# Kernel optimization log

Hardware: AMD Instinct MI355X
Metric: run time of the kernel (lower is better)

## Reference

```python
import jax, jax.numpy as jnp
import numpy as np

H, C = 4, 32  # heads, per-head channels
EPS = 1e-5


def setup_inputs() -> dict:
    key = jax.random.key(0)
    ks = jax.random.split(key, 12)
    N, E, IN = 100000, 1600000, 16
    lut_idx = jnp.arange(1024, dtype=jnp.int32)
    x = jax.random.normal(ks[0], (N, IN), dtype=jnp.float32)
    # LUT flag column: exactly the lut_idx nodes have value 1.0 (matches x[:,15]==1.0 mask)
    x = x.at[:, 15].set(0.0).at[lut_idx, 15].set(1.0)
    edge_index = jax.random.randint(ks[1], (2, E), 0, N, dtype=jnp.int64)
    s = 0.1
    return {
        "x": x,
        "edge_index": edge_index,
        "lut_idx": lut_idx,
        "W_lin": jax.random.normal(ks[2], (IN, H * C), dtype=jnp.float32) * s,
        "att_src": jax.random.normal(ks[3], (H, C), dtype=jnp.float32) * s,
        "att_dst": jax.random.normal(ks[4], (H, C), dtype=jnp.float32) * s,
        "bias_gat": jnp.zeros((H * C,), dtype=jnp.float32),
        "gamma": jnp.ones((H * C,), dtype=jnp.float32),
        "beta": jnp.zeros((H * C,), dtype=jnp.float32),
        "W1": jax.random.normal(ks[5], (H * C, 32), dtype=jnp.float32) * s,
        "b1": jnp.zeros((32,), dtype=jnp.float32),
        "W2": jax.random.normal(ks[6], (32, 1), dtype=jnp.float32) * s,
        "b2": jnp.zeros((1,), dtype=jnp.float32),
    }


def gat_conv(x, edge_index, W_lin, att_src, att_dst, bias_gat):
    N = x.shape[0]
    # add self-loops (PyG GATConv default)
    loops = jnp.arange(N, dtype=edge_index.dtype)
    src = jnp.concatenate([edge_index[0], loops])
    dst = jnp.concatenate([edge_index[1], loops])
    h = (x @ W_lin).reshape(N, H, C)                      # [N,H,C]
    a_src = (h * att_src[None]).sum(-1)                   # [N,H]
    a_dst = (h * att_dst[None]).sum(-1)                   # [N,H]
    e = jax.nn.leaky_relu(a_src[src] + a_dst[dst], 0.2)   # [Etot,H]
    m = jax.ops.segment_max(e, dst, num_segments=N)       # stable softmax per dst
    e = jnp.exp(e - m[dst])
    denom = jax.ops.segment_sum(e, dst, num_segments=N)
    alpha = e / denom[dst]                                # [Etot,H]
    msg = h[src] * alpha[:, :, None]                      # [Etot,H,C]
    out = jax.ops.segment_sum(msg, dst, num_segments=N)   # [N,H,C]
    return out.reshape(N, H * C) + bias_gat


def reference(x, edge_index, lut_idx, W_lin, att_src, att_dst, bias_gat,
              gamma, beta, W1, b1, W2, b2):
    h = gat_conv(x, edge_index, W_lin, att_src, att_dst, bias_gat)
    # BatchNorm over nodes (training-mode batch stats, biased var, eps=1e-5)
    mean = h.mean(axis=0)
    var = h.var(axis=0)
    h = (h - mean) / jnp.sqrt(var + EPS) * gamma + beta
    h = jax.nn.relu(h)
    emb = h[lut_idx]                                      # masked LUT nodes
    z = jax.nn.leaky_relu(emb @ W1 + b1, 0.01)            # Dropout is identity in eval
    out = z @ W2 + b2                                     # [n_lut, 1]
    return jnp.squeeze(out, axis=0) if out.shape[0] == 1 else out
```

## Files before the change

### kernel.cpp

```cpp
#include <hip/hip_runtime.h>
#include <hip/hip_fp16.h>
#include <cstdint>
#include <cstring>

typedef unsigned int uint;

#define BSHIFT 8
#define NBUCK 512
#define TILE 4096
#define SCAT_T 512
#define FUSE_T 1024
#define SORT_CAP 5120

__device__ __forceinline__ float leaky02(float x) { return x > 0.f ? x : 0.2f * x; }
__device__ __forceinline__ float bflo(uint u) { return __uint_as_float(u << 16); }
__device__ __forceinline__ float bfhi(uint u) { return __uint_as_float(u & 0xffff0000u); }

__device__ __forceinline__ uint pack_bf16x2(float a, float b) {
    uint ua = __float_as_uint(a), ub = __float_as_uint(b);
    ua += 0x7fffu + ((ua >> 16) & 1u);
    ub += 0x7fffu + ((ub >> 16) & 1u);
    return (ua >> 16) | (ub & 0xffff0000u);
}

__device__ __forceinline__ uint packh2(float a, float b) {
    __half ha = __float2half_rn(a), hb = __float2half_rn(b);
    unsigned short ua, ub;
    memcpy(&ua, &ha, 2);
    memcpy(&ub, &hb, 2);
    return (uint)ua | ((uint)ub << 16);
}

__device__ __forceinline__ float h2f_sel(uint2 xw, int head) {
    uint wrd = (head & 2) ? xw.y : xw.x;
    unsigned short us = (unsigned short)((head & 1) ? (wrd >> 16) : (wrd & 0xffffu));
    __half hh; memcpy(&hh, &us, 2);
    return __half2float(hh);
}

__global__ void k_linear(const float* __restrict__ x, const float* __restrict__ W,
                         const float* __restrict__ att_s, const float* __restrict__ att_d,
                         uint* __restrict__ h, float* __restrict__ a_src,
                         float* __restrict__ a_dst, int* __restrict__ cursor,
                         float* __restrict__ sums, float* __restrict__ sumsq,
                         unsigned char* __restrict__ flags, int N) {
    int tid = threadIdx.x;
    __shared__ float sx[32][16];
    __shared__ float sWs[64], sWd[64];
    int j = tid & 63;
    int sub = tid >> 6;
    int n0 = blockIdx.x * 32;

    if (blockIdx.x == 0) {
        cursor[tid] = 0; cursor[tid + 256] = 0;
        if (tid < 128) sums[tid] = 0.f;
        else sumsq[tid - 128] = 0.f;
    }
    if (tid < 32 && n0 + tid < N) flags[n0 + tid] = 0;

    float2 wreg[16];
#pragma unroll
    for (int k = 0; k < 16; k++) wreg[k] = ((const float2*)(W + k * 128))[j];

    if (tid < 128) {
        int row = tid >> 2;
        if (n0 + row < N)
            ((float4*)sx)[tid] = ((const float4*)(x + (size_t)n0 * 16))[tid];
    } else if (tid < 192) {
        int t = tid - 128;
        int k = t >> 2, hh = t & 3;
        float s1 = 0.f, s2 = 0.f;
        for (int c = 0; c < 32; c++) {
            float wv = W[k * 128 + hh * 32 + c];
            s1 += wv * att_s[hh * 32 + c];
            s2 += wv * att_d[hh * 32 + c];
        }
        sWs[t] = s1;
        sWd[t] = s2;
    }
    __syncthreads();

#pragma unroll
    for (int i = 0; i < 8; i++) {
        int loc = sub + i * 4;
        int n = n0 + loc;
        if (n >= N) break;
        float acc0 = 0.f, acc1 = 0.f;
#pragma unroll
        for (int k = 0; k < 16; k++) {
            float xk = sx[loc][k];
            acc0 += xk * wreg[k].x;
            acc1 += xk * wreg[k].y;
        }
        h[(size_t)n * 64 + j] = pack_bf16x2(acc0, acc1);
    }

    int loc2 = tid >> 3, hh = (tid >> 1) & 3, sd = tid & 1;
    int n2 = n0 + loc2;
    if (n2 < N) {
        const float* Wm = sd ? sWd : sWs;
        float acc = 0.f;
#pragma unroll
        for (int k = 0; k < 16; k++) acc += sx[loc2][k] * Wm[k * 4 + hh];
        if (sd) a_dst[n2 * 4 + hh] = acc;
        else    a_src[n2 * 4 + hh] = acc;
    }
}

__global__ void kb_scatter(const int* __restrict__ src, const int* __restrict__ dst, int E,
                           int* __restrict__ cursor, uint* __restrict__ pairs,
                           const int* __restrict__ lut, int nlut,
                           unsigned char* __restrict__ flags) {
    __shared__ int tileCnt[NBUCK], tileCnt2[NBUCK], tileOff[NBUCK], gbase[NBUCK];
    __shared__ int wsum[8], wbase[8];
    __shared__ uint lp[TILE];
    __shared__ unsigned short lb[TILE];
    int tid = threadIdx.x;
    int l = tid & 63, w = tid >> 6;
    int t0 = blockIdx.x * TILE;
    if (blockIdx.x == 0) {
        for (int k = tid; k < nlut; k += SCAT_T) flags[lut[k]] = 1;
    }
    tileCnt[tid] = 0;
    tileCnt2[tid] = 0;
    __syncthreads();
    int dreg[8], sreg[8];
#pragma unroll
    for (int j = 0; j < 8; j++) {
        int idx = t0 + j * SCAT_T + tid;
        if (idx < E) {
            dreg[j] = dst[idx];
            sreg[j] = src[idx];
            atomicAdd(&tileCnt[dreg[j] >> BSHIFT], 1);
        } else dreg[j] = -1;
    }
    __syncthreads();
    int v = tileCnt[tid];
    int s = v;
#pragma unroll
    for (int off = 1; off < 64; off <<= 1) {
        int t = __shfl_up(s, off);
        if (l >= off) s += t;
    }
    if (l == 63) wsum[w] = s;
    __syncthreads();
    if (tid < 8) {
        int b = 0;
        for (int i = 0; i < tid; i++) b += wsum[i];
        wbase[tid] = b;
    }
    __syncthreads();
    int ex = s - v + wbase[w];
    tileOff[tid] = ex;
    if (v > 0) gbase[tid] = atomicAdd(&cursor[tid], v);
    __syncthreads();
#pragma unroll
    for (int j = 0; j < 8; j++) {
        if (dreg[j] >= 0) {
            int bk = dreg[j] >> BSHIFT;
            int r = atomicAdd(&tileCnt2[bk], 1);
            int pos = tileOff[bk] + r;
            lp[pos] = ((uint)sreg[j] << BSHIFT) | (uint)(dreg[j] & 255);
            lb[pos] = (unsigned short)bk;
        }
    }
    __syncthreads();
    int tot = min(TILE, E - t0);
    for (int k = tid; k < tot; k += SCAT_T) {
        int bk = lb[k];
        int lpos = gbase[bk] + (k - tileOff[bk]);
        if (lpos < SORT_CAP)
            pairs[(size_t)bk * SORT_CAP + lpos] = lp[k];
    }
}

__global__ void __launch_bounds__(1024, 8) kb_sortgat(
                           const uint* __restrict__ pairs, const int* __restrict__ cursor,
                           const float* __restrict__ a_src, const float* __restrict__ a_dst,
                           const uint* __restrict__ h, const float* __restrict__ bias,
                           const unsigned char* __restrict__ flags,
                           uint* __restrict__ hagg,
                           float* __restrict__ sums, float* __restrict__ sumsq, int N) {
    __shared__ int cnt[256], off0[256], degl[256];
    __shared__ int wsum[4], wbase[4];
    __shared__ uint lcode[SORT_CAP];
    __shared__ uint2 wlds[SORT_CAP];
    __shared__ float4 sad[256];
    int tid = threadIdx.x;
    int l = tid & 63, w = tid >> 6;
    int b = blockIdx.x;
    int n0 = b << BSHIFT;
    int nn = min(256, N - n0);
    int ebase = b * SORT_CAP;
    int ecnt = cursor[b];
    if (ecnt > SORT_CAP) ecnt = SORT_CAP;
    if (tid < 256) cnt[tid] = 0;
    if (tid < nn) sad[tid] = ((const float4*)a_dst)[n0 + tid];
    __syncthreads();
    for (int k = tid; k < ecnt; k += FUSE_T)
        atomicAdd(&cnt[pairs[ebase + k] & 255], 1);
    __syncthreads();
    int v = (tid < 256) ? cnt[tid] : 0;
    int s = v;
#pragma unroll
    for (int off = 1; off < 64; off <<= 1) {
        int t = __shfl_up(s, off);
        if (l >= off) s += t;
    }
    if (tid < 256 && l == 63) wsum[w] = s;
    __syncthreads();
    if (tid < 4) {
        int base = 0;
        for (int i = 0; i < tid; i++) base += wsum[i];
        wbase[tid] = base;
    }
    __syncthreads();
    if (tid < 256) {
        off0[tid] = s - v + wbase[w];
        degl[tid] = v;
    }
    __syncthreads();
    if (tid < 256) cnt[tid] = 0;
    __syncthreads();
    for (int k = tid; k < ecnt; k += FUSE_T) {
        uint p = pairs[ebase + k];
        int ln = p & 255;
        int src = (int)(p >> BSHIFT);
        int r = atomicAdd(&cnt[ln], 1);
        int pos = off0[ln] + r;
        lcode[pos] = (uint)src;
        float4 as = ((const float4*)a_src)[src];
        float4 ad = sad[ln];
        wlds[pos] = make_uint2(
            packh2(__expf(leaky02(as.x + ad.x)), __expf(leaky02(as.y + ad.y))),
            packh2(__expf(leaky02(as.z + ad.z)), __expf(leaky02(as.w + ad.w))));
    }
    __syncthreads();
    int q = l >> 4;
    int l16 = l & 15;
    int head = l16 >> 2;
    float4 b0 = ((const float4*)bias)[2 * l16];
    float4 b1 = ((const float4*)bias)[2 * l16 + 1];
    float sv[8], sq[8];
#pragma unroll
    for (int j = 0; j < 8; j++) { sv[j] = 0.f; sq[j] = 0.f; }
    for (int pass = 0; pass < 4; pass++) {
        int ln = pass * 64 + w * 4 + q;
        if (ln >= nn) continue;
        int d = n0 + ln;
        int ebs = off0[ln];
        int deg = degl[ln];
        float asv = a_src[d * 4 + head];
        float adv = ((const float*)sad)[ln * 4 + head];
        float wslf = __expf(leaky02(asv + adv));
        uint4 u = ((const uint4*)(h + (size_t)d * 64))[l16];
        float sum = wslf;
        float2 a01 = make_float2(wslf * bflo(u.x), wslf * bfhi(u.x));
        float2 a23 = make_float2(wslf * bflo(u.y), wslf * bfhi(u.y));
        float2 a45 = make_float2(wslf * bflo(u.z), wslf * bfhi(u.z));
        float2 a67 = make_float2(wslf * bflo(u.w), wslf * bfhi(u.w));

        int i = 0;
        for (; i + 3 < deg; i += 4) {
            uint p0 = lcode[ebs + i];
            uint p1 = lcode[ebs + i + 1];
            uint p2 = lcode[ebs + i + 2];
            uint p3 = lcode[ebs + i + 3];
            uint2 x0 = wlds[ebs + i];
            uint2 x1 = wlds[ebs + i + 1];
            uint2 x2 = wlds[ebs + i + 2];
            uint2 x3 = wlds[ebs + i + 3];
            float w0 = h2f_sel(x0, head);
            float w1 = h2f_sel(x1, head);
            float w2 = h2f_sel(x2, head);
            float w3 = h2f_sel(x3, head);
            uint4 u0 = ((const uint4*)(h + (size_t)p0 * 64))[l16];
            uint4 u1 = ((const uint4*)(h + (size_t)p1 * 64))[l16];
            uint4 u2 = ((const uint4*)(h + (size_t)p2 * 64))[l16];
            uint4 u3 = ((const uint4*)(h + (size_t)p3 * 64))[l16];
            sum += (w0 + w1) + (w2 + w3);
            float2 w02 = {w0, w0}, w12 = {w1, w1}, w22 = {w2, w2}, w32 = {w3, w3};
            a01 += make_float2(bflo(u0.x), bfhi(u0.x)) * w02
                 + make_float2(bflo(u1.x), bfhi(u1.x)) * w12
                 + make_float2(bflo(u2.x), bfhi(u2.x)) * w22
                 + make_float2(bflo(u3.x), bfhi(u3.x)) * w32;
            a23 += make_float2(bflo(u0.y), bfhi(u0.y)) * w02
                 + make_float2(bflo(u1.y), bfhi(u1.y)) * w12
                 + make_float2(bflo(u2.y), bfhi(u2.y)) * w22
                 + make_float2(bflo(u3.y), bfhi(u3.y)) * w32;
            a45 += make_float2(bflo(u0.z), bfhi(u0.z)) * w02
                 + make_float2(bflo(u1.z), bfhi(u1.z)) * w12
                 + make_float2(bflo(u2.z), bfhi(u2.z)) * w22
                 + make_float2(bflo(u3.z), bfhi(u3.z)) * w32;
            a67 += make_float2(bflo(u0.w), bfhi(u0.w)) * w02
                 + make_float2(bflo(u1.w), bfhi(u1.w)) * w12
                 + make_float2(bflo(u2.w), bfhi(u2.w)) * w22
                 + make_float2(bflo(u3.w), bfhi(u3.w)) * w32;
        }
        for (; i < deg; i++) {
            uint p0 = lcode[ebs + i];
            float w0 = h2f_sel(wlds[ebs + i], head);
            uint4 u0 = ((const uint4*)(h + (size_t)p0 * 64))[l16];
            sum += w0;
            float2 w02 = {w0, w0};
            a01 += make_float2(bflo(u0.x), bfhi(u0.x)) * w02;
            a23 += make_float2(bflo(u0.y), bfhi(u0.y)) * w02;
            a45 += make_float2(bflo(u0.z), bfhi(u0.z)) * w02;
            a67 += make_float2(bflo(u0.w), bfhi(u0.w)) * w02;
        }
        float inv = 1.f / sum;
        float v0 = a01.x * inv + b0.x;
        float v1 = a01.y * inv + b0.y;
        float v2 = a23.x * inv + b0.z;
        float v3 = a23.y * inv + b0.w;
        float v4 = a45.x * inv + b1.x;
        float v5 = a45.y * inv + b1.y;
        float v6 = a67.x * inv + b1.z;
        float v7 = a67.y * inv + b1.w;
        sv[0] += v0; sq[0] += v0 * v0;
        sv[1] += v1; sq[1] += v1 * v1;
        sv[2] += v2; sq[2] += v2 * v2;
        sv[3] += v3; sq[3] += v3 * v3;
        sv[4] += v4; sq[4] += v4 * v4;
        sv[5] += v5; sq[5] += v5 * v5;
        sv[6] += v6; sq[6] += v6 * v6;
        sv[7] += v7; sq[7] += v7 * v7;
        if (flags[d]) {
            uint4 o;
            o.x = pack_bf16x2(v0, v1);
            o.y = pack_bf16x2(v2, v3);
            o.z = pack_bf16x2(v4, v5);
            o.w = pack_bf16x2(v6, v7);
            ((uint4*)(hagg + (size_t)d * 64))[l16] = o;
        }
    }
    __syncthreads();
#pragma unroll
    for (int j = 0; j < 8; j++) {
        sv[j] += __shfl_xor(sv[j], 16);
        sv[j] += __shfl_xor(sv[j], 32);
        sq[j] += __shfl_xor(sq[j], 16);
        sq[j] += __shfl_xor(sq[j], 32);
    }
    float* red = (float*)lcode;
    if (l < 16) {
#pragma unroll
        for (int j = 0; j < 8; j++) {
            red[(w * 16 + l) * 16 + j] = sv[j];
            red[(w * 16 + l) * 16 + 8 + j] = sq[j];
        }
    }
    __syncthreads();
    if (tid < 256) {
        int lg = tid >> 4, j = tid & 15;
        float tot = 0.f;
#pragma unroll
        for (int ww = 0; ww < 16; ww++) tot += red[(ww * 16 + lg) * 16 + j];
        if (j < 8) atomicAdd(&sums[lg * 8 + j], tot);
        else       atomicAdd(&sumsq[lg * 8 + j - 8], tot);
    }
}

__global__ void k_mlp(const uint* __restrict__ hagg, const int* __restrict__ lut,
                      const float* __restrict__ sums, const float* __restrict__ sumsq,
                      const float* __restrict__ gamma, const float* __restrict__ beta,
                      const float* __restrict__ W1, const float* __restrict__ b1,
                      const float* __restrict__ W2, const float* __restrict__ b2,
                      float* __restrict__ out, int N, int nlut) {
    int blk = blockIdx.x;
    if (blk >= nlut) return;
    int node = lut[blk];
    int lane = threadIdx.x;
    __shared__ float v[128];
    float invN = 1.f / (float)N;
    uint u = hagg[(size_t)node * 64 + lane];
    int c0 = 2 * lane, c1 = 2 * lane + 1;
    {
        float mean = sums[c0] * invN;
        float var = sumsq[c0] * invN - mean * mean;
        float val = (bflo(u) - mean) / sqrtf(var + 1e-5f) * gamma[c0] + beta[c0];
        v[c0] = fmaxf(val, 0.f);
        mean = sums[c1] * invN;
        var = sumsq[c1] * invN - mean * mean;
        val = (bfhi(u) - mean) / sqrtf(var + 1e-5f) * gamma[c1] + beta[c1];
        v[c1] = fmaxf(val, 0.f);
    }
    __syncthreads();
    float r = 0.f;
    if (lane < 32) {
        float z = b1[lane];
        for (int c = 0; c < 128; c++) z += v[c] * W1[c * 32 + lane];
        z = z > 0.f ? z : 0.01f * z;
        r = z * W2[lane];
    }
#pragma unroll
    for (int off = 16; off >= 1; off >>= 1) r += __shfl_xor(r, off);
    if (lane == 0) out[blk] = r + b2[0];
}

extern "C" void kernel_launch(void* const* d_in, const int* in_sizes, int n_in,
                              void* d_out, int out_size, void* d_ws, size_t ws_size,
                              hipStream_t stream) {
    const float* x     = (const float*)d_in[0];
    const int*   edges = (const int*)d_in[1];
    const int*   lut   = (const int*)d_in[2];
    const float* W_lin = (const float*)d_in[3];
    const float* att_s = (const float*)d_in[4];
    const float* att_d = (const float*)d_in[5];
    const float* bias  = (const float*)d_in[6];
    const float* gamma = (const float*)d_in[7];
    const float* beta  = (const float*)d_in[8];
    const float* W1    = (const float*)d_in[9];
    const float* b1    = (const float*)d_in[10];
    const float* W2    = (const float*)d_in[11];
    const float* b2    = (const float*)d_in[12];

    int N = in_sizes[0] / 16;
    int E = in_sizes[1] / 2;
    int nlut = in_sizes[2];
    int B = (N + 255) >> BSHIFT;

    const int* esrc = edges;
    const int* edst = edges + E;

    char* ws = (char*)d_ws;
    size_t off = 0;
    auto alloc = [&](size_t bytes) -> void* {
        void* p = ws + off;
        off += (bytes + 255) & ~(size_t)255;
        return p;
    };
    uint*  h       = (uint*)alloc((size_t)N * 64 * 4);
    uint*  hagg    = (uint*)alloc((size_t)N * 64 * 4);
    float* a_src   = (float*)alloc((size_t)N * 4 * 4);
    float* a_dst   = (float*)alloc((size_t)N * 4 * 4);
    uint*  pairs   = (uint*)alloc((size_t)B * SORT_CAP * 4);
    int*   cursor  = (int*)alloc((size_t)NBUCK * 4);
    float* sums    = (float*)alloc(128 * 4);
    float* sumsq   = (float*)alloc(128 * 4);
    unsigned char* flags = (unsigned char*)alloc((size_t)N);

    k_linear<<<(N + 31) / 32, 256, 0, stream>>>(x, W_lin, att_s, att_d, h,
                                                a_src, a_dst, cursor, sums, sumsq,
                                                flags, N);
    kb_scatter<<<(E + TILE - 1) / TILE, SCAT_T, 0, stream>>>(esrc, edst, E, cursor, pairs,
                                                             lut, nlut, flags);
    kb_sortgat<<<B, FUSE_T, 0, stream>>>(pairs, cursor, a_src, a_dst, h, bias,
                                         flags, hagg, sums, sumsq, N);
    k_mlp<<<nlut, 64, 0, stream>>>(hagg, lut, sums, sumsq, gamma, beta, W1, b1, W2, b2,
                                   (float*)d_out, N, nlut);
}
```

Baseline: 211.3 us.

## Fuse linear and edge-scatter kernels into one launch, zero buffers via memset

Merges the node linear projection and the edge bucket-scatter into a single kernel whose blocks branch on blockIdx, so the two independent phases run concurrently in one launch instead of two serialized ones. Zeroing of cursor, sums and flags moves into a hipMemsetAsync, since the scatter blocks can no longer rely on a prior kernel to clear them. The sort/aggregate kernel also stages the bias in shared memory and cuts the gather unroll from 4 to 2 to ease register pressure. The merged kernel uses a larger shared-memory footprint per block, and the linear part now handles 64 nodes per 512-thread block.

After: 190.5 us. 9.8% less time.

```diff
diff --git a/kernel.cpp b/kernel.cpp
--- a/kernel.cpp
+++ b/kernel.cpp
@@ -8,8 +8,8 @@
 #define BSHIFT 8
 #define NBUCK 512
 #define TILE 4096
-#define SCAT_T 512
 #define FUSE_T 1024
+#define LS_T 512
 #define SORT_CAP 5120
 
 __device__ __forceinline__ float leaky02(float x) { return x > 0.f ? x : 0.2f * x; }
@@ -38,139 +38,131 @@
     return __half2float(hh);
 }
 
-__global__ void k_linear(const float* __restrict__ x, const float* __restrict__ W,
-                         const float* __restrict__ att_s, const float* __restrict__ att_d,
-                         uint* __restrict__ h, float* __restrict__ a_src,
-                         float* __restrict__ a_dst, int* __restrict__ cursor,
-                         float* __restrict__ sums, float* __restrict__ sumsq,
-                         unsigned char* __restrict__ flags, int N) {
+__global__ void k_linscat(const float* __restrict__ x, const float* __restrict__ W,
+                          const float* __restrict__ att_s, const float* __restrict__ att_d,
+                          uint* __restrict__ h, float* __restrict__ a_src,
+                          float* __restrict__ a_dst,
+                          const int* __restrict__ src, const int* __restrict__ dst, int E,
+                          int* __restrict__ cursor, uint* __restrict__ pairs,
+                          const int* __restrict__ lut, int nlut,
+                          unsigned char* __restrict__ flags, int N, int Lb) {
     int tid = threadIdx.x;
-    __shared__ float sx[32][16];
-    __shared__ float sWs[64], sWd[64];
-    int j = tid & 63;
-    int sub = tid >> 6;
-    int n0 = blockIdx.x * 32;
-
-    if (blockIdx.x == 0) {
-        cursor[tid] = 0; cursor[tid + 256] = 0;
-        if (tid < 128) sums[tid] = 0.f;
-        else sumsq[tid - 128] = 0.f;
-    }
-    if (tid < 32 && n0 + tid < N) flags[n0 + tid] = 0;
-
-    float2 wreg[16];
-#pragma unroll
-    for (int k = 0; k < 16; k++) wreg[k] = ((const float2*)(W + k * 128))[j];
-
-    if (tid < 128) {
-        int row = tid >> 2;
-        if (n0 + row < N)
-            ((float4*)sx)[tid] = ((const float4*)(x + (size_t)n0 * 16))[tid];
-    } else if (tid < 192) {
-        int t = tid - 128;
-        int k = t >> 2, hh = t & 3;
-        float s1 = 0.f, s2 = 0.f;
-        for (int c = 0; c < 32; c++) {
-            float wv = W[k * 128 + hh * 32 + c];
-            s1 += wv * att_s[hh * 32 + c];
-            s2 += wv * att_d[hh * 32 + c];
-        }
-        sWs[t] = s1;
-        sWd[t] = s2;
-    }
-    __syncthreads();
-
-#pragma unroll
-    for (int i = 0; i < 8; i++) {
-        int loc = sub + i * 4;
-        int n = n0 + loc;
-        if (n >= N) break;
-        float acc0 = 0.f, acc1 = 0.f;
-#pragma unroll
-        for (int k = 0; k < 16; k++) {
-            float xk = sx[loc][k];
-            acc0 += xk * wreg[k].x;
-            acc1 += xk * wreg[k].y;
-        }
-        h[(size_t)n * 64 + j] = pack_bf16x2(acc0, acc1);
-    }
-
-    int loc2 = tid >> 3, hh = (tid >> 1) & 3, sd = tid & 1;
-    int n2 = n0 + loc2;
-    if (n2 < N) {
-        const float* Wm = sd ? sWd : sWs;
-        float acc = 0.f;
-#pragma unroll
-        for (int k = 0; k < 16; k++) acc += sx[loc2][k] * Wm[k * 4 + hh];
-        if (sd) a_dst[n2 * 4 + hh] = acc;
-        else    a_src[n2 * 4 + hh] = acc;
-    }
-}
-
-__global__ void kb_scatter(const int* __restrict__ src, const int* __restrict__ dst, int E,
-                           int* __restrict__ cursor, uint* __restrict__ pairs,
-                           const int* __restrict__ lut, int nlut,
-                           unsigned char* __restrict__ flags) {
-    __shared__ int tileCnt[NBUCK], tileCnt2[NBUCK], tileOff[NBUCK], gbase[NBUCK];
-    __shared__ int wsum[8], wbase[8];
-    __shared__ uint lp[TILE];
-    __shared__ unsigned short lb[TILE];
-    int tid = threadIdx.x;
-    int l = tid & 63, w = tid >> 6;
-    int t0 = blockIdx.x * TILE;
-    if (blockIdx.x == 0) {
-        for (int k = tid; k < nlut; k += SCAT_T) flags[lut[k]] = 1;
-    }
-    tileCnt[tid] = 0;
-    tileCnt2[tid] = 0;
-    __syncthreads();
-    int dreg[8], sreg[8];
-#pragma unroll
-    for (int j = 0; j < 8; j++) {
-        int idx = t0 + j * SCAT_T + tid;
-        if (idx < E) {
-            dreg[j] = dst[idx];
-            sreg[j] = src[idx];
-            atomicAdd(&tileCnt[dreg[j] >> BSHIFT], 1);
-        } else dreg[j] = -1;
-    }
-    __syncthreads();
-    int v = tileCnt[tid];
-    int s = v;
-#pragma unroll
-    for (int off = 1; off < 64; off <<= 1) {
-        int t = __shfl_up(s, off);
-        if (l >= off) s += t;
-    }
-    if (l == 63) wsum[w] = s;
-    __syncthreads();
-    if (tid < 8) {
-        int b = 0;
-        for (int i = 0; i < tid; i++) b += wsum[i];
-        wbase[tid] = b;
-    }
-    __syncthreads();
-    int ex = s - v + wbase[w];
-    tileOff[tid] = ex;
-    if (v > 0) gbase[tid] = atomicAdd(&cursor[tid], v);
-    __syncthreads();
-#pragma unroll
-    for (int j = 0; j < 8; j++) {
-        if (dreg[j] >= 0) {
-            int bk = dreg[j] >> BSHIFT;
-            int r = atomicAdd(&tileCnt2[bk], 1);
-            int pos = tileOff[bk] + r;
-            lp[pos] = ((uint)sreg[j] << BSHIFT) | (uint)(dreg[j] & 255);
-            lb[pos] = (unsigned short)bk;
-        }
-    }
-    __syncthreads();
-    int tot = min(TILE, E - t0);
-    for (int k = tid; k < tot; k += SCAT_T) {
-        int bk = lb[k];
-        int lpos = gbase[bk] + (k - tileOff[bk]);
-        if (lpos < SORT_CAP)
-            pairs[(size_t)bk * SORT_CAP + lpos] = lp[k];
+    if (blockIdx.x < Lb) {
+        __shared__ float sx[64][16];
+        __shared__ float sWs[64], sWd[64];
+        int j = tid & 63;
+        int sub = tid >> 6;
+        int n0 = blockIdx.x * 64;
+
+        float2 wreg[16];
+#pragma unroll
+        for (int k = 0; k < 16; k++) wreg[k] = ((const float2*)(W + k * 128))[j];
+
+        if (tid < 256) {
+            int row = tid >> 2;
+            if (n0 + row < N)
+                ((float4*)sx)[tid] = ((const float4*)(x + (size_t)n0 * 16))[tid];
+        } else if (tid < 320) {
+            int t = tid - 256;
+            int k = t >> 2, hh = t & 3;
+            float s1 = 0.f, s2 = 0.f;
+            for (int c = 0; c < 32; c++) {
+                float wv = W[k * 128 + hh * 32 + c];
+                s1 += wv * att_s[hh * 32 + c];
+                s2 += wv * att_d[hh * 32 + c];
+            }
+            sWs[t] = s1;
+            sWd[t] = s2;
+        }
+        __syncthreads();
+
+#pragma unroll
+        for (int i = 0; i < 8; i++) {
+            int loc = sub + i * 8;
+            int n = n0 + loc;
+            if (n >= N) break;
+            float acc0 = 0.f, acc1 = 0.f;
+#pragma unroll
+            for (int k = 0; k < 16; k++) {
+                float xk = sx[loc][k];
+                acc0 += xk * wreg[k].x;
+                acc1 += xk * wreg[k].y;
+            }
+            h[(size_t)n * 64 + j] = pack_bf16x2(acc0, acc1);
+        }
+
+        int loc2 = tid >> 3, hh = (tid >> 1) & 3, sd = tid & 1;
+        int n2 = n0 + loc2;
+        if (n2 < N) {
+            const float* Wm = sd ? sWd : sWs;
+            float acc = 0.f;
+#pragma unroll
+            for (int k = 0; k < 16; k++) acc += sx[loc2][k] * Wm[k * 4 + hh];
+            if (sd) a_dst[n2 * 4 + hh] = acc;
+            else    a_src[n2 * 4 + hh] = acc;
+        }
+    } else {
+        __shared__ int tileCnt[NBUCK], tileCnt2[NBUCK], tileOff[NBUCK], gbase[NBUCK];
+        __shared__ int wsum[8], wbase[8];
+        __shared__ uint lp[TILE];
+        __shared__ unsigned short lb[TILE];
+        int bid = blockIdx.x - Lb;
+        int l = tid & 63, w = tid >> 6;
+        int t0 = bid * TILE;
+        if (bid == 0) {
+            for (int k = tid; k < nlut; k += LS_T) flags[lut[k]] = 1;
+        }
+        tileCnt[tid] = 0;
+        tileCnt2[tid] = 0;
+        __syncthreads();
+        int dreg[8], sreg[8];
+#pragma unroll
+        for (int jj = 0; jj < 8; jj++) {
+            int idx = t0 + jj * LS_T + tid;
+            if (idx < E) {
+                dreg[jj] = dst[idx];
+                sreg[jj] = src[idx];
+                atomicAdd(&tileCnt[dreg[jj] >> BSHIFT], 1);
+            } else dreg[jj] = -1;
+        }
+        __syncthreads();
+        int v = tileCnt[tid];
+        int s = v;
+#pragma unroll
+        for (int off = 1; off < 64; off <<= 1) {
+            int t = __shfl_up(s, off);
+            if (l >= off) s += t;
+        }
+        if (l == 63) wsum[w] = s;
+        __syncthreads();
+        if (tid < 8) {
+            int b = 0;
+            for (int i = 0; i < tid; i++) b += wsum[i];
+            wbase[tid] = b;
+        }
+        __syncthreads();
+        int ex = s - v + wbase[w];
+        tileOff[tid] = ex;
+        if (v > 0) gbase[tid] = atomicAdd(&cursor[tid], v);
+        __syncthreads();
+#pragma unroll
+        for (int jj = 0; jj < 8; jj++) {
+            if (dreg[jj] >= 0) {
+                int bk = dreg[jj] >> BSHIFT;
+                int r = atomicAdd(&tileCnt2[bk], 1);
+                int pos = tileOff[bk] + r;
+                lp[pos] = ((uint)sreg[jj] << BSHIFT) | (uint)(dreg[jj] & 255);
+                lb[pos] = (unsigned short)bk;
+            }
+        }
+        __syncthreads();
+        int tot = min(TILE, E - t0);
+        for (int k = tid; k < tot; k += LS_T) {
+            int bk = lb[k];
+            int lpos = gbase[bk] + (k - tileOff[bk]);
+            if (lpos < SORT_CAP)
+                pairs[(size_t)bk * SORT_CAP + lpos] = lp[k];
+        }
     }
 }
 
@@ -186,6 +178,7 @@
     __shared__ uint lcode[SORT_CAP];
     __shared__ uint2 wlds[SORT_CAP];
     __shared__ float4 sad[256];
+    __shared__ float4 sbias[32];
     int tid = threadIdx.x;
     int l = tid & 63, w = tid >> 6;
     int b = blockIdx.x;
@@ -196,6 +189,7 @@
     if (ecnt > SORT_CAP) ecnt = SORT_CAP;
     if (tid < 256) cnt[tid] = 0;
     if (tid < nn) sad[tid] = ((const float4*)a_dst)[n0 + tid];
+    if (tid >= 992) sbias[tid - 992] = ((const float4*)bias)[tid - 992];
     __syncthreads();
     for (int k = tid; k < ecnt; k += FUSE_T)
         atomicAdd(&cnt[pairs[ebase + k] & 255], 1);
@@ -239,8 +233,6 @@
     int q = l >> 4;
     int l16 = l & 15;
     int head = l16 >> 2;
-    float4 b0 = ((const float4*)bias)[2 * l16];
-    float4 b1 = ((const float4*)bias)[2 * l16 + 1];
     float sv[8], sq[8];
 #pragma unroll
     for (int j = 0; j < 8; j++) { sv[j] = 0.f; sq[j] = 0.f; }
@@ -261,43 +253,25 @@
         float2 a67 = make_float2(wslf * bflo(u.w), wslf * bfhi(u.w));
 
         int i = 0;
-        for (; i + 3 < deg; i += 4) {
+        for (; i + 1 < deg; i += 2) {
             uint p0 = lcode[ebs + i];
             uint p1 = lcode[ebs + i + 1];
-            uint p2 = lcode[ebs + i + 2];
-            uint p3 = lcode[ebs + i + 3];
-            uint2 x0 = wlds[ebs + i];
-            uint2 x1 = wlds[ebs + i + 1];
-            uint2 x2 = wlds[ebs + i + 2];
-            uint2 x3 = wlds[ebs + i + 3];
-            float w0 = h2f_sel(x0, head);
-            float w1 = h2f_sel(x1, head);
-            float w2 = h2f_sel(x2, head);
-            float w3 = h2f_sel(x3, head);
+            float w0 = h2f_sel(wlds[ebs + i], head);
+            float w1 = h2f_sel(wlds[ebs + i + 1], head);
             uint4 u0 = ((const uint4*)(h + (size_t)p0 * 64))[l16];
             uint4 u1 = ((const uint4*)(h + (size_t)p1 * 64))[l16];
-            uint4 u2 = ((const uint4*)(h + (size_t)p2 * 64))[l16];
-            uint4 u3 = ((const uint4*)(h + (size_t)p3 * 64))[l16];
-            sum += (w0 + w1) + (w2 + w3);
-            float2 w02 = {w0, w0}, w12 = {w1, w1}, w22 = {w2, w2}, w32 = {w3, w3};
+            sum += w0 + w1;
+            float2 w02 = {w0, w0}, w12 = {w1, w1};
             a01 += make_float2(bflo(u0.x), bfhi(u0.x)) * w02
-                 + make_float2(bflo(u1.x), bfhi(u1.x)) * w12
-                 + make_float2(bflo(u2.x), bfhi(u2.x)) * w22
-                 + make_float2(bflo(u3.x), bfhi(u3.x)) * w32;
+                 + make_float2(bflo(u1.x), bfhi(u1.x)) * w12;
             a23 += make_float2(bflo(u0.y), bfhi(u0.y)) * w02
-                 + make_float2(bflo(u1.y), bfhi(u1.y)) * w12
-                 + make_float2(bflo(u2.y), bfhi(u2.y)) * w22
-                 + make_float2(bflo(u3.y), bfhi(u3.y)) * w32;
+                 + make_float2(bflo(u1.y), bfhi(u1.y)) * w12;
             a45 += make_float2(bflo(u0.z), bfhi(u0.z)) * w02
-                 + make_float2(bflo(u1.z), bfhi(u1.z)) * w12
-                 + make_float2(bflo(u2.z), bfhi(u2.z)) * w22
-                 + make_float2(bflo(u3.z), bfhi(u3.z)) * w32;
+                 + make_float2(bflo(u1.z), bfhi(u1.z)) * w12;
             a67 += make_float2(bflo(u0.w), bfhi(u0.w)) * w02
-                 + make_float2(bflo(u1.w), bfhi(u1.w)) * w12
-                 + make_float2(bflo(u2.w), bfhi(u2.w)) * w22
-                 + make_float2(bflo(u3.w), bfhi(u3.w)) * w32;
-        }
-        for (; i < deg; i++) {
+                 + make_float2(bflo(u1.w), bfhi(u1.w)) * w12;
+        }
+        if (i < deg) {
             uint p0 = lcode[ebs + i];
             float w0 = h2f_sel(wlds[ebs + i], head);
             uint4 u0 = ((const uint4*)(h + (size_t)p0 * 64))[l16];
@@ -309,6 +283,8 @@
             a67 += make_float2(bflo(u0.w), bfhi(u0.w)) * w02;
         }
         float inv = 1.f / sum;
+        float4 b0 = sbias[2 * l16];
+        float4 b1 = sbias[2 * l16 + 1];
         float v0 = a01.x * inv + b0.x;
         float v1 = a01.y * inv + b0.y;
         float v2 = a23.x * inv + b0.z;
@@ -419,6 +395,8 @@
     int E = in_sizes[1] / 2;
     int nlut = in_sizes[2];
     int B = (N + 255) >> BSHIFT;
+    int Lb = (N + 63) / 64;
+    int Sb = (E + TILE - 1) / TILE;
 
     const int* esrc = edges;
     const int* edst = edges + E;
@@ -435,16 +413,17 @@
     float* a_src   = (float*)alloc((size_t)N * 4 * 4);
     float* a_dst   = (float*)alloc((size_t)N * 4 * 4);
     uint*  pairs   = (uint*)alloc((size_t)B * SORT_CAP * 4);
+    char*  zbase   = ws + off;
     int*   cursor  = (int*)alloc((size_t)NBUCK * 4);
     float* sums    = (float*)alloc(128 * 4);
     float* sumsq   = (float*)alloc(128 * 4);
     unsigned char* flags = (unsigned char*)alloc((size_t)N);
-
-    k_linear<<<(N + 31) / 32, 256, 0, stream>>>(x, W_lin, att_s, att_d, h,
-                                                a_src, a_dst, cursor, sums, sumsq,
-                                                flags, N);
-    kb_scatter<<<(E + TILE - 1) / TILE, SCAT_T, 0, stream>>>(esrc, edst, E, cursor, pairs,
-                                                             lut, nlut, flags);
+    size_t zspan = (size_t)((ws + off) - zbase);
+
+    hipMemsetAsync(zbase, 0, zspan, stream);
+    k_linscat<<<Lb + Sb, LS_T, 0, stream>>>(x, W_lin, att_s, att_d, h, a_src, a_dst,
+                                            esrc, edst, E, cursor, pairs,
+                                            lut, nlut, flags, N, Lb);
     kb_sortgat<<<B, FUSE_T, 0, stream>>>(pairs, cursor, a_src, a_dst, h, bias,
                                          flags, hagg, sums, sumsq, N);
     k_mlp<<<nlut, 64, 0, stream>>>(hagg, lut, sums, sumsq, gamma, beta, W1, b1, W2, b2,
```
